# Performance work log

Measured on AMD Instinct MI355X. Metric: run time of the kernel, lower is better.

## Reference

```python
import jax, jax.numpy as jnp
import numpy as np

N_NODES = 100000
N_EDGES = 1600000
IN_C, HID_C, OUT_C = 128, 128, 128


def setup_inputs() -> dict:
    key = jax.random.key(0)
    k_x, k_e, k_w1, k_w2 = jax.random.split(key, 4)
    x = jax.random.normal(k_x, (N_NODES, IN_C), dtype=jnp.float32)
    edge_index = jax.random.randint(k_e, (2, N_EDGES), 0, N_NODES, dtype=jnp.int64)
    # Glorot-style init for GCNConv linear weights
    s1 = (6.0 / (IN_C + HID_C)) ** 0.5
    s2 = (6.0 / (HID_C + OUT_C)) ** 0.5
    W1 = jax.random.uniform(k_w1, (IN_C, HID_C), jnp.float32, -s1, s1)
    b1 = jnp.zeros((HID_C,), jnp.float32)
    W2 = jax.random.uniform(k_w2, (HID_C, OUT_C), jnp.float32, -s2, s2)
    b2 = jnp.zeros((OUT_C,), jnp.float32)
    return {"x": x, "edge_index": edge_index, "W1": W1, "b1": b1, "W2": W2, "b2": b2}


def gcn_conv(x, src, dst, W, b, num_nodes):
    # PyG GCNConv: linear transform, then sym-normalized aggregation with self-loops.
    h = x @ W                                   # [N, out]
    ones = jnp.ones_like(dst, dtype=h.dtype)
    # degree counts include the self-loop (+1)
    deg = jax.ops.segment_sum(ones, dst, num_segments=num_nodes) + 1.0
    inv_sqrt = jax.lax.rsqrt(deg)               # deg > 0 since self-loops
    coef = inv_sqrt[src] * inv_sqrt[dst]        # [E]
    msgs = h[src] * coef[:, None]               # [E, out] gather + scale
    agg = jax.ops.segment_sum(msgs, dst, num_segments=num_nodes)
    # self-loop contribution: coef = 1/deg for the (i,i) edge
    agg = agg + h * (inv_sqrt * inv_sqrt)[:, None]
    return agg + b


def reference(x, edge_index, W1, b1, W2, b2):
    src, dst = edge_index[0], edge_index[1]
    h = gcn_conv(x, src, dst, W1, b1, N_NODES)
    h = jax.nn.relu(h)
    out = gcn_conv(h, src, dst, W2, b2, N_NODES)
    return out
```

## Files before the change

kernel.cpp:

```cpp
#include <hip/hip_runtime.h>
#include <hip/hip_bf16.h>
#include <hip/hip_fp16.h>

#define N_NODES 100000
#define N_EDGES 1600000
#define C 128
#define NB 782
#define NC 256
#define EPC (N_EDGES / NC)

typedef _Float16 half8 __attribute__((ext_vector_type(8)));
typedef _Float16 half4v __attribute__((ext_vector_type(4)));
typedef float f32x4 __attribute__((ext_vector_type(4)));

__global__ __launch_bounds__(256) void init_count(const float* __restrict__ W1,
                                                  const float* __restrict__ W2,
                                                  _Float16* __restrict__ W1s,
                                                  _Float16* __restrict__ W2s,
                                                  const int* __restrict__ dst,
                                                  int* __restrict__ cnt) {
    __shared__ int hist[NB];
    if (blockIdx.x < 16) {
        int i = blockIdx.x * 256 + threadIdx.x;
        int which = i >> 11;
        int u = i & 2047;
        int lane = u & 63, l = lane & 15, q = lane >> 4;
        int ct = u >> 6, c = ct >> 3, t = ct & 7;
        const float* Wsrc = which ? W2 : W1;
        _Float16* Dst = which ? W2s : W1s;
        half8 v;
#pragma unroll
        for (int j = 0; j < 8; j++)
            v[j] = (_Float16)Wsrc[(c * 32 + q * 8 + j) * C + t * 16 + l];
        *(half8*)(Dst + (size_t)u * 8) = v;
    } else {
        int c = blockIdx.x - 16;
        int tid = threadIdx.x;
        for (int b = tid; b < NB; b += 256) hist[b] = 0;
        __syncthreads();
        int base = c * EPC;
        for (int i = tid; i < EPC; i += 256)
            atomicAdd(&hist[dst[base + i] >> 7], 1);
        __syncthreads();
        for (int b = tid; b < NB; b += 256) cnt[b * NC + c] = hist[b];
    }
}

__global__ __launch_bounds__(256) void scan_block2(int* __restrict__ a,
                                                   int* __restrict__ partial, int n) {
    __shared__ int s[256];
    int tid = threadIdx.x;
    int i = blockIdx.x * 256 + tid;
    int v = (i < n) ? a[i] : 0;
    s[tid] = v;
    __syncthreads();
    for (int off = 1; off < 256; off <<= 1) {
        int t = (tid >= off) ? s[tid - off] : 0;
        __syncthreads();
        s[tid] += t;
        __syncthreads();
    }
    if (i < n) a[i] = s[tid] - v;
    if (tid == 255) partial[blockIdx.x] = s[255];
}

__global__ __launch_bounds__(1024) void scan_partial_1024(int* __restrict__ partial, int n) {
    __shared__ int s[1024];
    int tid = threadIdx.x;
    int v = (tid < n) ? partial[tid] : 0;
    s[tid] = v;
    __syncthreads();
    for (int off = 1; off < 1024; off <<= 1) {
        int t = (tid >= off) ? s[tid - off] : 0;
        __syncthreads();
        s[tid] += t;
        __syncthreads();
    }
    if (tid < n) partial[tid] = s[tid] - v;
}

__global__ __launch_bounds__(256) void scan_add(int* __restrict__ a,
                                                const int* __restrict__ partial, int n) {
    int i = blockIdx.x * 256 + threadIdx.x;
    if (i < n) a[i] += partial[blockIdx.x];
}

template <typename T>
__device__ __forceinline__ void gemm_body(const T* __restrict__ A,
                                          const _Float16* __restrict__ Wsw,
                                          _Float16* __restrict__ out, int n,
                                          int bid, int tid, _Float16* smem) {
    int lane = tid & 63;
    int w = tid >> 6;
    int m0 = bid * 64;

    if constexpr (sizeof(T) == 4) {
        const float4* A4 = (const float4*)A;
#pragma unroll
        for (int p = 0; p < 8; p++) {
            int idx = p * 256 + tid;
            int r = idx >> 5, f4 = idx & 31;
            int row = m0 + r; if (row >= n) row = n - 1;
            float4 v = A4[(size_t)row * 32 + f4];
            int kg = f4 >> 1, hi = f4 & 1;
            half4v hv = {(_Float16)v.x, (_Float16)v.y, (_Float16)v.z, (_Float16)v.w};
            *(half4v*)(smem + r * 128 + ((kg ^ (r & 15)) * 8) + hi * 4) = hv;
        }
    } else {
#pragma unroll
        for (int p = 0; p < 4; p++) {
            int idx = p * 256 + tid;
            int r = idx >> 4, kg = idx & 15;
            int row = m0 + r; if (row >= n) row = n - 1;
            half8 v = *(const half8*)(A + (size_t)row * C + kg * 8);
            *(half8*)(smem + r * 128 + ((kg ^ (r & 15)) * 8)) = v;
        }
    }
    __syncthreads();

    int l = lane & 15, q = lane >> 4;
    f32x4 acc[8] = {};

#pragma unroll
    for (int c = 0; c < 4; c++) {
        half8 af = *(const half8*)(smem + (w * 16 + l) * 128 + (((c * 4 + q) ^ l) * 8));
#pragma unroll
        for (int t = 0; t < 8; t++) {
            half8 bf = *(const half8*)(Wsw + (size_t)((c * 8 + t) * 64 + lane) * 8);
            acc[t] = __builtin_amdgcn_mfma_f32_16x16x32_f16(af, bf, acc[t], 0, 0, 0);
        }
    }

    __syncthreads();
    _Float16* cb = smem + w * 2176;
#pragma unroll
    for (int t = 0; t < 8; t++)
#pragma unroll
        for (int i = 0; i < 4; i++)
            cb[(q * 4 + i) * 136 + t * 16 + l] = (_Float16)acc[t][i];
    __syncthreads();
#pragma unroll
    for (int i = 0; i < 4; i++) {
        int r16 = i * 4 + q;
        int row = m0 + w * 16 + r16;
        if (row < n)
            *(half8*)(out + (size_t)row * C + l * 8) =
                *(const half8*)(cb + r16 * 136 + l * 8);
    }
}

template <typename T>
__global__ __launch_bounds__(256) void gemm_mfma(const T* __restrict__ A,
                                                 const _Float16* __restrict__ Wsw,
                                                 _Float16* __restrict__ out, int n) {
    __shared__ _Float16 smem[8704];
    gemm_body<T>(A, Wsw, out, n, blockIdx.x, threadIdx.x, smem);
}

__global__ __launch_bounds__(256) void fused_gemm_scatter(const float* __restrict__ x,
                                                          const _Float16* __restrict__ W1s,
                                                          _Float16* __restrict__ h16, int n,
                                                          const int* __restrict__ src,
                                                          const int* __restrict__ dst,
                                                          const int* __restrict__ S,
                                                          long long* __restrict__ bsorted,
                                                          int nbG) {
    __shared__ _Float16 smem[8704];
    if ((int)blockIdx.x < nbG) {
        gemm_body<float>(x, W1s, h16, n, blockIdx.x, threadIdx.x, smem);
    } else {
        int c = blockIdx.x - nbG;
        int tid = threadIdx.x;
        int* off = (int*)smem;
        for (int b = tid; b < NB; b += 256) off[b] = S[b * NC + c];
        __syncthreads();
        int base = c * EPC;
        for (int i = tid; i < EPC; i += 256) {
            int s = src[base + i];
            int d = dst[base + i];
            int p = atomicAdd(&off[d >> 7], 1);
            bsorted[p] = ((long long)(unsigned long long)(unsigned int)d << 32) |
                         (unsigned int)s;
        }
    }
}

__global__ __launch_bounds__(256) void node_sort(const long long* __restrict__ bsorted,
                                                 const int* __restrict__ S,
                                                 long long* __restrict__ final2,
                                                 int* __restrict__ rowptr,
                                                 float* __restrict__ isq) {
    __shared__ int hist[128];
    __shared__ int sc[128];
    __shared__ int off2[128];
    __shared__ float iqb[128];
    int b = blockIdx.x, tid = threadIdx.x;
    int beg = S[b * NC];
    int end = (b == NB - 1) ? N_EDGES : S[(b + 1) * NC];
    if (tid < 128) hist[tid] = 0;
    __syncthreads();
    for (int i = beg + tid; i < end; i += 256) {
        int d = (int)((unsigned long long)bsorted[i] >> 32);
        atomicAdd(&hist[d & 127], 1);
    }
    __syncthreads();
    if (tid < 128) sc[tid] = hist[tid];
    __syncthreads();
    for (int off = 1; off < 128; off <<= 1) {
        int t = 0;
        if (tid < 128 && tid >= off) t = sc[tid - off];
        __syncthreads();
        if (tid < 128) sc[tid] += t;
        __syncthreads();
    }
    if (tid < 128) {
        int node = b * 128 + tid;
        int deg = hist[tid];
        int start = beg + sc[tid] - deg;
        off2[tid] = start;
        if (node < N_NODES) {
            rowptr[node] = start;
            float iq = rsqrtf((float)deg + 1.0f);
            isq[node] = iq;
            iqb[tid] = iq;
        }
    }
    if (b == 0 && tid == 0) rowptr[N_NODES] = N_EDGES;
    __syncthreads();
    for (int i = beg + tid; i < end; i += 256) {
        long long rec = bsorted[i];
        int d = (int)((unsigned long long)rec >> 32);
        int li = d & 127;
        int p = atomicAdd(&off2[li], 1);
        final2[p] = ((long long)(unsigned long long)__float_as_uint(iqb[li]) << 32) |
                    (unsigned int)(rec & 0xffffffffLL);
    }
}

__global__ __launch_bounds__(256) void coef_fill(const long long* __restrict__ final2,
                                                 const float* __restrict__ isq,
                                                 long long* __restrict__ edges, int E) {
    int i = blockIdx.x * 256 + threadIdx.x;
    if (i < E) {
        long long rec = final2[i];
        int s = (int)(rec & 0xffffffffLL);
        float iqd = __uint_as_float((unsigned int)((unsigned long long)rec >> 32));
        float cf = isq[s] * iqd;
        long long orec = ((long long)(unsigned long long)__float_as_uint(cf) << 32) |
                         (unsigned int)s;
        __builtin_nontemporal_store(orec, &edges[i]);
    }
}

template <bool RELU, typename OT>
__global__ __launch_bounds__(256) void aggregate(const _Float16* __restrict__ h,
                                                 const int* __restrict__ rowptr,
                                                 const long long* __restrict__ edges,
                                                 const float* __restrict__ isq,
                                                 const float* __restrict__ bias,
                                                 OT* __restrict__ out, int n) {
    int lane = threadIdx.x & 63;
    int wave = threadIdx.x >> 6;
    int node = blockIdx.x * 4 + wave;
    if (node >= n) return;

    int q   = lane >> 4;
    int l16 = lane & 15;
    int cb  = l16 * 8;

    int beg = rowptr[node];
    int end = rowptr[node + 1];

    float acc[8] = {};

    int j = beg + q;
    for (; j + 12 < end; j += 16) {
        unsigned long long e0 = (unsigned long long)edges[j];
        unsigned long long e1 = (unsigned long long)edges[j + 4];
        unsigned long long e2 = (unsigned long long)edges[j + 8];
        unsigned long long e3 = (unsigned long long)edges[j + 12];
        half8 h0 = *(const half8*)(h + (size_t)(unsigned int)e0 * C + cb);
        half8 h1 = *(const half8*)(h + (size_t)(unsigned int)e1 * C + cb);
        half8 h2 = *(const half8*)(h + (size_t)(unsigned int)e2 * C + cb);
        half8 h3 = *(const half8*)(h + (size_t)(unsigned int)e3 * C + cb);
        float c0 = __uint_as_float((unsigned int)(e0 >> 32));
        float c1 = __uint_as_float((unsigned int)(e1 >> 32));
        float c2 = __uint_as_float((unsigned int)(e2 >> 32));
        float c3 = __uint_as_float((unsigned int)(e3 >> 32));
#pragma unroll
        for (int k = 0; k < 8; k++) acc[k] += c0 * (float)h0[k];
#pragma unroll
        for (int k = 0; k < 8; k++) acc[k] += c1 * (float)h1[k];
#pragma unroll
        for (int k = 0; k < 8; k++) acc[k] += c2 * (float)h2[k];
#pragma unroll
        for (int k = 0; k < 8; k++) acc[k] += c3 * (float)h3[k];
    }
    for (; j < end; j += 4) {
        unsigned long long e = (unsigned long long)edges[j];
        half8 hv = *(const half8*)(h + (size_t)(unsigned int)e * C + cb);
        float cf = __uint_as_float((unsigned int)(e >> 32));
#pragma unroll
        for (int k = 0; k < 8; k++) acc[k] += cf * (float)hv[k];
    }

#pragma unroll
    for (int k = 0; k < 8; k++) {
        acc[k] += __shfl_xor(acc[k], 16, 64);
        acc[k] += __shfl_xor(acc[k], 32, 64);
    }

    if (q == 0) {
        float invd = isq[node];
        float sc = invd * invd;
        half8 hd = *(const half8*)(h + (size_t)node * C + cb);
        float4 bv0 = *(const float4*)(bias + cb);
        float4 bv1 = *(const float4*)(bias + cb + 4);
        float bb[8] = {bv0.x, bv0.y, bv0.z, bv0.w, bv1.x, bv1.y, bv1.z, bv1.w};
#pragma unroll
        for (int k = 0; k < 8; k++) {
            acc[k] += sc * (float)hd[k] + bb[k];
            if (RELU) acc[k] = fmaxf(acc[k], 0.f);
        }
        if constexpr (sizeof(OT) == 2) {
            half8 o;
#pragma unroll
            for (int k = 0; k < 8; k++) o[k] = (_Float16)acc[k];
            *(half8*)((_Float16*)out + (size_t)node * C + cb) = o;
        } else {
            float4 o0 = {acc[0], acc[1], acc[2], acc[3]};
            float4 o1 = {acc[4], acc[5], acc[6], acc[7]};
            *(float4*)((float*)out + (size_t)node * C + cb) = o0;
            *(float4*)((float*)out + (size_t)node * C + cb + 4) = o1;
        }
    }
}

extern "C" void kernel_launch(void* const* d_in, const int* in_sizes, int n_in,
                              void* d_out, int out_size, void* d_ws, size_t ws_size,
                              hipStream_t stream) {
    const float* x  = (const float*)d_in[0];
    const int* ei   = (const int*)d_in[1];
    const float* W1 = (const float*)d_in[2];
    const float* b1 = (const float*)d_in[3];
    const float* W2 = (const float*)d_in[4];
    const float* b2 = (const float*)d_in[5];
    float* out = (float*)d_out;

    const int N = N_NODES, E = N_EDGES;
    const int* src = ei;
    const int* dst = ei + E;

    char* ws = (char*)d_ws;
    size_t off = 0;
    auto alloc = [&](size_t bytes) {
        size_t o = off;
        off = (off + bytes + 255) & ~(size_t)255;
        return o;
    };
    _Float16* h16   = (_Float16*)(ws + alloc((size_t)N * C * 2));
    _Float16* hB16  = (_Float16*)(ws + alloc((size_t)N * C * 2));
    _Float16* W1s   = (_Float16*)(ws + alloc((size_t)C * C * 2));
    _Float16* W2s   = (_Float16*)(ws + alloc((size_t)C * C * 2));
    int*      cnt   = (int*)     (ws + alloc((size_t)NB * NC * 4));
    int*      part  = (int*)     (ws + alloc((size_t)1024 * 4));
    long long* ebuf1 = (long long*)(ws + alloc((size_t)E * 8));
    long long* ebuf2 = (long long*)(ws + alloc((size_t)E * 8));
    int*    rowptr  = (int*)     (ws + alloc((size_t)(N + 1) * 4));
    float*    isq   = (float*)   (ws + alloc((size_t)N * 4));
    (void)ws_size; (void)n_in; (void)in_sizes; (void)out_size;

    const int nbG = (N + 63) / 64;
    const int nS  = NB * NC;
    const int nbS = nS / 256;
    const int nbE = (E + 255) / 256;

    init_count<<<16 + NC, 256, 0, stream>>>(W1, W2, W1s, W2s, dst, cnt);

    scan_block2<<<nbS, 256, 0, stream>>>(cnt, part, nS);
    scan_partial_1024<<<1, 1024, 0, stream>>>(part, nbS);
    scan_add<<<nbS, 256, 0, stream>>>(cnt, part, nS);

    fused_gemm_scatter<<<nbG + NC, 256, 0, stream>>>(x, W1s, h16, N, src, dst, cnt,
                                                     ebuf1, nbG);

    node_sort<<<NB, 256, 0, stream>>>(ebuf1, cnt, ebuf2, rowptr, isq);

    coef_fill<<<nbE, 256, 0, stream>>>(ebuf2, isq, ebuf1, E);

    aggregate<true, _Float16><<<(N + 3) / 4, 256, 0, stream>>>(h16, rowptr, ebuf1, isq, b1, hB16, N);

    gemm_mfma<_Float16><<<nbG, 256, 0, stream>>>(hB16, W2s, h16, N);

    aggregate<false, float><<<(N + 3) / 4, 256, 0, stream>>>(h16, rowptr, ebuf1, isq, b2, out, N);
}
```

Before: 339.0 us.

## Pack edge records to 32-bit, drop coef_fill, fuse layer-1 aggregation into GEMM2

Edge records shrink from 64-bit (dst,src) pairs to a 32-bit packed local-dst/src word, and the final CSR stores only source ids. Edge coefficients are recomputed on the fly from isq[src]*isq[dst] instead of being written by a separate coef_fill pass. The layer-1 aggregate+ReLU now writes rows straight into shared memory and is followed by the second GEMM in one kernel, which removes one launch and one N×C fp16 round trip. The cost is an extra random isq gather per edge, and the fused kernel runs only 4 waves per 64 rows serially over 16 nodes each, so it has less parallelism than the old per-node aggregate.

```diff
diff --git a/kernel.cpp b/kernel.cpp
--- a/kernel.cpp
+++ b/kernel.cpp
@@ -85,17 +85,55 @@
     if (i < n) a[i] += partial[blockIdx.x];
 }
 
-template <typename T>
-__device__ __forceinline__ void gemm_body(const T* __restrict__ A,
-                                          const _Float16* __restrict__ Wsw,
-                                          _Float16* __restrict__ out, int n,
-                                          int bid, int tid, _Float16* smem) {
+__device__ __forceinline__ void gemm_compute_store(const _Float16* __restrict__ Wsw,
+                                                   _Float16* __restrict__ out, int n,
+                                                   int m0, int tid, _Float16* smem) {
     int lane = tid & 63;
     int w = tid >> 6;
-    int m0 = bid * 64;
-
-    if constexpr (sizeof(T) == 4) {
-        const float4* A4 = (const float4*)A;
+    int l = lane & 15, q = lane >> 4;
+    f32x4 acc[8] = {};
+
+#pragma unroll
+    for (int c = 0; c < 4; c++) {
+        half8 af = *(const half8*)(smem + (w * 16 + l) * 128 + (((c * 4 + q) ^ l) * 8));
+#pragma unroll
+        for (int t = 0; t < 8; t++) {
+            half8 bf = *(const half8*)(Wsw + (size_t)((c * 8 + t) * 64 + lane) * 8);
+            acc[t] = __builtin_amdgcn_mfma_f32_16x16x32_f16(af, bf, acc[t], 0, 0, 0);
+        }
+    }
+
+    __syncthreads();
+    _Float16* cbuf = smem + w * 2176;
+#pragma unroll
+    for (int t = 0; t < 8; t++)
+#pragma unroll
+        for (int i = 0; i < 4; i++)
+            cbuf[(q * 4 + i) * 136 + t * 16 + l] = (_Float16)acc[t][i];
+    __syncthreads();
+#pragma unroll
+    for (int i = 0; i < 4; i++) {
+        int r16 = i * 4 + q;
+        int row = m0 + w * 16 + r16;
+        if (row < n)
+            *(half8*)(out + (size_t)row * C + l * 8) =
+                *(const half8*)(cbuf + r16 * 136 + l * 8);
+    }
+}
+
+__global__ __launch_bounds__(256) void fused_gemm_scatter(const float* __restrict__ x,
+                                                          const _Float16* __restrict__ W1s,
+                                                          _Float16* __restrict__ h16, int n,
+                                                          const int* __restrict__ src,
+                                                          const int* __restrict__ dst,
+                                                          const int* __restrict__ S,
+                                                          unsigned int* __restrict__ bpacked,
+                                                          int nbG) {
+    __shared__ _Float16 smem[8704];
+    if ((int)blockIdx.x < nbG) {
+        int tid = threadIdx.x;
+        int m0 = blockIdx.x * 64;
+        const float4* A4 = (const float4*)x;
 #pragma unroll
         for (int p = 0; p < 8; p++) {
             int idx = p * 256 + tid;
@@ -106,68 +144,8 @@
             half4v hv = {(_Float16)v.x, (_Float16)v.y, (_Float16)v.z, (_Float16)v.w};
             *(half4v*)(smem + r * 128 + ((kg ^ (r & 15)) * 8) + hi * 4) = hv;
         }
-    } else {
-#pragma unroll
-        for (int p = 0; p < 4; p++) {
-            int idx = p * 256 + tid;
-            int r = idx >> 4, kg = idx & 15;
-            int row = m0 + r; if (row >= n) row = n - 1;
-            half8 v = *(const half8*)(A + (size_t)row * C + kg * 8);
-            *(half8*)(smem + r * 128 + ((kg ^ (r & 15)) * 8)) = v;
-        }
-    }
-    __syncthreads();
-
-    int l = lane & 15, q = lane >> 4;
-    f32x4 acc[8] = {};
-
-#pragma unroll
-    for (int c = 0; c < 4; c++) {
-        half8 af = *(const half8*)(smem + (w * 16 + l) * 128 + (((c * 4 + q) ^ l) * 8));
-#pragma unroll
-        for (int t = 0; t < 8; t++) {
-            half8 bf = *(const half8*)(Wsw + (size_t)((c * 8 + t) * 64 + lane) * 8);
-            acc[t] = __builtin_amdgcn_mfma_f32_16x16x32_f16(af, bf, acc[t], 0, 0, 0);
-        }
-    }
-
-    __syncthreads();
-    _Float16* cb = smem + w * 2176;
-#pragma unroll
-    for (int t = 0; t < 8; t++)
-#pragma unroll
-        for (int i = 0; i < 4; i++)
-            cb[(q * 4 + i) * 136 + t * 16 + l] = (_Float16)acc[t][i];
-    __syncthreads();
-#pragma unroll
-    for (int i = 0; i < 4; i++) {
-        int r16 = i * 4 + q;
-        int row = m0 + w * 16 + r16;
-        if (row < n)
-            *(half8*)(out + (size_t)row * C + l * 8) =
-                *(const half8*)(cb + r16 * 136 + l * 8);
-    }
-}
-
-template <typename T>
-__global__ __launch_bounds__(256) void gemm_mfma(const T* __restrict__ A,
-                                                 const _Float16* __restrict__ Wsw,
-                                                 _Float16* __restrict__ out, int n) {
-    __shared__ _Float16 smem[8704];
-    gemm_body<T>(A, Wsw, out, n, blockIdx.x, threadIdx.x, smem);
-}
-
-__global__ __launch_bounds__(256) void fused_gemm_scatter(const float* __restrict__ x,
-                                                          const _Float16* __restrict__ W1s,
-                                                          _Float16* __restrict__ h16, int n,
-                                                          const int* __restrict__ src,
-                                                          const int* __restrict__ dst,
-                                                          const int* __restrict__ S,
-                                                          long long* __restrict__ bsorted,
-                                                          int nbG) {
-    __shared__ _Float16 smem[8704];
-    if ((int)blockIdx.x < nbG) {
-        gemm_body<float>(x, W1s, h16, n, blockIdx.x, threadIdx.x, smem);
+        __syncthreads();
+        gemm_compute_store(W1s, h16, n, m0, tid, smem);
     } else {
         int c = blockIdx.x - nbG;
         int tid = threadIdx.x;
@@ -179,30 +157,26 @@
             int s = src[base + i];
             int d = dst[base + i];
             int p = atomicAdd(&off[d >> 7], 1);
-            bsorted[p] = ((long long)(unsigned long long)(unsigned int)d << 32) |
-                         (unsigned int)s;
-        }
-    }
-}
-
-__global__ __launch_bounds__(256) void node_sort(const long long* __restrict__ bsorted,
+            bpacked[p] = ((unsigned int)(d & 127) << 17) | (unsigned int)s;
+        }
+    }
+}
+
+__global__ __launch_bounds__(256) void node_sort(const unsigned int* __restrict__ bpacked,
                                                  const int* __restrict__ S,
-                                                 long long* __restrict__ final2,
+                                                 int* __restrict__ srcs,
                                                  int* __restrict__ rowptr,
                                                  float* __restrict__ isq) {
     __shared__ int hist[128];
     __shared__ int sc[128];
     __shared__ int off2[128];
-    __shared__ float iqb[128];
     int b = blockIdx.x, tid = threadIdx.x;
     int beg = S[b * NC];
     int end = (b == NB - 1) ? N_EDGES : S[(b + 1) * NC];
     if (tid < 128) hist[tid] = 0;
     __syncthreads();
-    for (int i = beg + tid; i < end; i += 256) {
-        int d = (int)((unsigned long long)bsorted[i] >> 32);
-        atomicAdd(&hist[d & 127], 1);
-    }
+    for (int i = beg + tid; i < end; i += 256)
+        atomicAdd(&hist[bpacked[i] >> 17], 1);
     __syncthreads();
     if (tid < 128) sc[tid] = hist[tid];
     __syncthreads();
@@ -220,42 +194,100 @@
         off2[tid] = start;
         if (node < N_NODES) {
             rowptr[node] = start;
-            float iq = rsqrtf((float)deg + 1.0f);
-            isq[node] = iq;
-            iqb[tid] = iq;
+            isq[node] = rsqrtf((float)deg + 1.0f);
         }
     }
     if (b == 0 && tid == 0) rowptr[N_NODES] = N_EDGES;
     __syncthreads();
     for (int i = beg + tid; i < end; i += 256) {
-        long long rec = bsorted[i];
-        int d = (int)((unsigned long long)rec >> 32);
-        int li = d & 127;
+        unsigned int rec = bpacked[i];
+        int li = (int)(rec >> 17);
         int p = atomicAdd(&off2[li], 1);
-        final2[p] = ((long long)(unsigned long long)__float_as_uint(iqb[li]) << 32) |
-                    (unsigned int)(rec & 0xffffffffLL);
-    }
-}
-
-__global__ __launch_bounds__(256) void coef_fill(const long long* __restrict__ final2,
-                                                 const float* __restrict__ isq,
-                                                 long long* __restrict__ edges, int E) {
-    int i = blockIdx.x * 256 + threadIdx.x;
-    if (i < E) {
-        long long rec = final2[i];
-        int s = (int)(rec & 0xffffffffLL);
-        float iqd = __uint_as_float((unsigned int)((unsigned long long)rec >> 32));
-        float cf = isq[s] * iqd;
-        long long orec = ((long long)(unsigned long long)__float_as_uint(cf) << 32) |
-                         (unsigned int)s;
-        __builtin_nontemporal_store(orec, &edges[i]);
-    }
+        srcs[p] = (int)(rec & 0x1FFFFu);
+    }
+}
+
+__global__ __launch_bounds__(256) void fused_agg_gemm(const _Float16* __restrict__ h,
+                                                      const int* __restrict__ rowptr,
+                                                      const int* __restrict__ srcs,
+                                                      const float* __restrict__ isq,
+                                                      const float* __restrict__ bias,
+                                                      const _Float16* __restrict__ Wsw,
+                                                      _Float16* __restrict__ out, int n) {
+    __shared__ _Float16 smem[8704];
+    int tid = threadIdx.x;
+    int lane = tid & 63, w = tid >> 6;
+    int q = lane >> 4, l16 = lane & 15;
+    int cb = l16 * 8;
+    int m0 = blockIdx.x * 64;
+
+    float4 bv0 = *(const float4*)(bias + cb);
+    float4 bv1 = *(const float4*)(bias + cb + 4);
+    float bb[8] = {bv0.x, bv0.y, bv0.z, bv0.w, bv1.x, bv1.y, bv1.z, bv1.w};
+
+#pragma unroll 1
+    for (int t = 0; t < 16; t++) {
+        int node = m0 + w * 16 + t;
+        if (node >= n) node = n - 1;
+        int beg = rowptr[node];
+        int end = rowptr[node + 1];
+        float iqd = isq[node];
+
+        float acc[8] = {};
+        int j = beg + q;
+        for (; j + 12 < end; j += 16) {
+            int s0 = srcs[j], s1 = srcs[j + 4], s2 = srcs[j + 8], s3 = srcs[j + 12];
+            half8 h0 = *(const half8*)(h + (size_t)s0 * C + cb);
+            half8 h1 = *(const half8*)(h + (size_t)s1 * C + cb);
+            half8 h2 = *(const half8*)(h + (size_t)s2 * C + cb);
+            half8 h3 = *(const half8*)(h + (size_t)s3 * C + cb);
+            float c0 = isq[s0] * iqd;
+            float c1 = isq[s1] * iqd;
+            float c2 = isq[s2] * iqd;
+            float c3 = isq[s3] * iqd;
+#pragma unroll
+            for (int k = 0; k < 8; k++) acc[k] += c0 * (float)h0[k];
+#pragma unroll
+            for (int k = 0; k < 8; k++) acc[k] += c1 * (float)h1[k];
+#pragma unroll
+            for (int k = 0; k < 8; k++) acc[k] += c2 * (float)h2[k];
+#pragma unroll
+            for (int k = 0; k < 8; k++) acc[k] += c3 * (float)h3[k];
+        }
+        for (; j < end; j += 4) {
+            int s = srcs[j];
+            half8 hv = *(const half8*)(h + (size_t)s * C + cb);
+            float cf = isq[s] * iqd;
+#pragma unroll
+            for (int k = 0; k < 8; k++) acc[k] += cf * (float)hv[k];
+        }
+
+#pragma unroll
+        for (int k = 0; k < 8; k++) {
+            acc[k] += __shfl_xor(acc[k], 16, 64);
+            acc[k] += __shfl_xor(acc[k], 32, 64);
+        }
+
+        if (q == 0) {
+            float sc = iqd * iqd;
+            half8 hd = *(const half8*)(h + (size_t)node * C + cb);
+            half8 o;
+#pragma unroll
+            for (int k = 0; k < 8; k++) {
+                float vv = acc[k] + sc * (float)hd[k] + bb[k];
+                o[k] = (_Float16)fmaxf(vv, 0.f);
+            }
+            int r = w * 16 + t;
+            *(half8*)(smem + r * 128 + ((l16 ^ t) * 8)) = o;
+        }
+    }
+    gemm_compute_store(Wsw, out, n, m0, tid, smem);
 }
 
 template <bool RELU, typename OT>
 __global__ __launch_bounds__(256) void aggregate(const _Float16* __restrict__ h,
                                                  const int* __restrict__ rowptr,
-                                                 const long long* __restrict__ edges,
+                                                 const int* __restrict__ srcs,
                                                  const float* __restrict__ isq,
                                                  const float* __restrict__ bias,
                                                  OT* __restrict__ out, int n) {
@@ -270,23 +302,21 @@
 
     int beg = rowptr[node];
     int end = rowptr[node + 1];
+    float iqd = isq[node];
 
     float acc[8] = {};
 
     int j = beg + q;
     for (; j + 12 < end; j += 16) {
-        unsigned long long e0 = (unsigned long long)edges[j];
-        unsigned long long e1 = (unsigned long long)edges[j + 4];
-        unsigned long long e2 = (unsigned long long)edges[j + 8];
-        unsigned long long e3 = (unsigned long long)edges[j + 12];
-        half8 h0 = *(const half8*)(h + (size_t)(unsigned int)e0 * C + cb);
-        half8 h1 = *(const half8*)(h + (size_t)(unsigned int)e1 * C + cb);
-        half8 h2 = *(const half8*)(h + (size_t)(unsigned int)e2 * C + cb);
-        half8 h3 = *(const half8*)(h + (size_t)(unsigned int)e3 * C + cb);
-        float c0 = __uint_as_float((unsigned int)(e0 >> 32));
-        float c1 = __uint_as_float((unsigned int)(e1 >> 32));
-        float c2 = __uint_as_float((unsigned int)(e2 >> 32));
-        float c3 = __uint_as_float((unsigned int)(e3 >> 32));
+        int s0 = srcs[j], s1 = srcs[j + 4], s2 = srcs[j + 8], s3 = srcs[j + 12];
+        half8 h0 = *(const half8*)(h + (size_t)s0 * C + cb);
+        half8 h1 = *(const half8*)(h + (size_t)s1 * C + cb);
+        half8 h2 = *(const half8*)(h + (size_t)s2 * C + cb);
+        half8 h3 = *(const half8*)(h + (size_t)s3 * C + cb);
+        float c0 = isq[s0] * iqd;
+        float c1 = isq[s1] * iqd;
+        float c2 = isq[s2] * iqd;
+        float c3 = isq[s3] * iqd;
 #pragma unroll
         for (int k = 0; k < 8; k++) acc[k] += c0 * (float)h0[k];
 #pragma unroll
@@ -297,9 +327,9 @@
         for (int k = 0; k < 8; k++) acc[k] += c3 * (float)h3[k];
     }
     for (; j < end; j += 4) {
-        unsigned long long e = (unsigned long long)edges[j];
-        half8 hv = *(const half8*)(h + (size_t)(unsigned int)e * C + cb);
-        float cf = __uint_as_float((unsigned int)(e >> 32));
+        int s = srcs[j];
+        half8 hv = *(const half8*)(h + (size_t)s * C + cb);
+        float cf = isq[s] * iqd;
 #pragma unroll
         for (int k = 0; k < 8; k++) acc[k] += cf * (float)hv[k];
     }
@@ -311,8 +341,7 @@
     }
 
     if (q == 0) {
-        float invd = isq[node];
-        float sc = invd * invd;
+        float sc = iqd * iqd;
         half8 hd = *(const half8*)(h + (size_t)node * C + cb);
         float4 bv0 = *(const float4*)(bias + cb);
         float4 bv1 = *(const float4*)(bias + cb + 4);
@@ -364,8 +393,8 @@
     _Float16* W2s   = (_Float16*)(ws + alloc((size_t)C * C * 2));
     int*      cnt   = (int*)     (ws + alloc((size_t)NB * NC * 4));
     int*      part  = (int*)     (ws + alloc((size_t)1024 * 4));
-    long long* ebuf1 = (long long*)(ws + alloc((size_t)E * 8));
-    long long* ebuf2 = (long long*)(ws + alloc((size_t)E * 8));
+    unsigned int* bpacked = (unsigned int*)(ws + alloc((size_t)E * 4));
+    int*      srcs  = (int*)     (ws + alloc((size_t)E * 4));
     int*    rowptr  = (int*)     (ws + alloc((size_t)(N + 1) * 4));
     float*    isq   = (float*)   (ws + alloc((size_t)N * 4));
     (void)ws_size; (void)n_in; (void)in_sizes; (void)out_size;
@@ -373,7 +402,6 @@
     const int nbG = (N + 63) / 64;
     const int nS  = NB * NC;
     const int nbS = nS / 256;
-    const int nbE = (E + 255) / 256;
 
     init_count<<<16 + NC, 256, 0, stream>>>(W1, W2, W1s, W2s, dst, cnt);
 
@@ -382,15 +410,11 @@
     scan_add<<<nbS, 256, 0, stream>>>(cnt, part, nS);
 
     fused_gemm_scatter<<<nbG + NC, 256, 0, stream>>>(x, W1s, h16, N, src, dst, cnt,
-                                                     ebuf1, nbG);
-
-    node_sort<<<NB, 256, 0, stream>>>(ebuf1, cnt, ebuf2, rowptr, isq);
-
-    coef_fill<<<nbE, 256, 0, stream>>>(ebuf2, isq, ebuf1, E);
-
-    aggregate<true, _Float16><<<(N + 3) / 4, 256, 0, stream>>>(h16, rowptr, ebuf1, isq, b1, hB16, N);
-
-    gemm_mfma<_Float16><<<nbG, 256, 0, stream>>>(hB16, W2s, h16, N);
-
-    aggregate<false, float><<<(N + 3) / 4, 256, 0, stream>>>(h16, rowptr, ebuf1, isq, b2, out, N);
-}
+                                                     bpacked, nbG);
+
+    node_sort<<<NB, 256, 0, stream>>>(bpacked, cnt, srcs, rowptr, isq);
+
+    fused_agg_gemm<<<nbG, 256, 0, stream>>>(h16, rowptr, srcs, isq, b1, W2s, hB16, N);
+
+    aggregate<false, float><<<(N + 3) / 4, 256, 0, stream>>>(hB16, rowptr, srcs, isq, b2, out, N);
+}
```

New measurement: 346.8 us. 1.02x slower.
